# Performance work log

Measured on AMD Instinct MI355X. Metric: run time of the kernel, lower is better.

Reference implementation:

```python
import jax, jax.numpy as jnp
import numpy as np
import math

BS, C, H, W, D = 2, 64, 32, 16, 32
FLAT = H * W * D          # 16384 voxels
N = 2048                  # non-empty voxels per sample (fixed for jit)
K = 256                   # min(int(0.2 * N), max_k=256)
EPS = 1e-5


def _pe(c, length):
    # sinusoidal positional encoding, interleaved sin/cos as in the torch code
    pos = jnp.arange(length, dtype=jnp.float32)[:, None]
    div = jnp.exp(jnp.arange(0, c, 2, dtype=jnp.float32) * (-math.log(10000.0) / c))
    ang = pos * div[None, :]                     # [length, c//2]
    return jnp.stack([jnp.sin(ang), jnp.cos(ang)], axis=-1).reshape(length, c)


def _bn(z, g, b):
    # eval-mode BatchNorm1d with running_mean=0, running_var=1
    return z * (g / jnp.sqrt(1.0 + EPS)) + b


def setup_inputs() -> dict:
    key = jax.random.key(0)
    ks = jax.random.split(key, 8)
    rng = np.random.default_rng(0)
    mask_idx = np.stack([np.sort(rng.choice(FLAT, size=N, replace=False)) for _ in range(BS)])
    w = lambda k, s: jax.random.normal(k, s, jnp.float32) * 0.05
    return dict(
        input=jax.random.normal(ks[0], (BS, C, H, W, D), jnp.float32),
        mask_idx=jnp.asarray(mask_idx, jnp.int32),
        w_ne1=w(ks[1], (C, 32)), b_ne1=jnp.zeros(32), g_ne=jnp.ones(32), be_ne=jnp.zeros(32),
        w_ne2=w(ks[2], (32, 1)), b_ne2=jnp.zeros(1),
        w_p1=w(ks[3], (C, 32)), b_p1=jnp.zeros(32), g_p1=jnp.ones(32), be_p1=jnp.zeros(32),
        w_p2=w(ks[4], (32, 32)), b_p2=jnp.zeros(32), g_p2=jnp.ones(32), be_p2=jnp.zeros(32),
        w_p3=w(ks[5], (32, 1)), b_p3=jnp.zeros(1),
        w_r1=w(ks[6], (4 * C, 2 * C)), b_r1=jnp.zeros(2 * C),
        w_r2=w(ks[7], (2 * C, C)), b_r2=jnp.zeros(C),
    )


def reference(input, mask_idx, w_ne1, b_ne1, g_ne, be_ne, w_ne2, b_ne2,
              w_p1, b_p1, g_p1, be_p1, w_p2, b_p2, g_p2, be_p2, w_p3, b_p3,
              w_r1, b_r1, w_r2, b_r2):
    bs, c = input.shape[0], input.shape[1]
    pe = _pe(c, FLAT)
    x = input                         # agg (external Bottleneck3D stack) ~ identity
    x_flat = x.reshape(bs, c, FLAT)

    def per_sample(xf, idx, key):
        mpe = pe[idx]                                  # [N, c] masked positional enc
        xi = xf[:, idx].T + mpe                        # [N, c] masked gather
        h1 = jax.nn.relu(_bn(xi @ w_ne1 + b_ne1, g_ne, be_ne))
        prob = jax.nn.sigmoid((h1 @ w_ne2 + b_ne2)[:, 0])    # [N] non-empty prob
        # torch.multinomial(prob, K, replacement=True)
        topk = jax.random.categorical(key, jnp.log(prob), shape=(K,))
        tf = xi[topk]                                  # [K, c] sampled features
        ne_k = prob[topk]                              # [K]
        # xi_repeat + tiled masked_pe[topk]  ->  [N, K, c]
        xw = xi[:, None, :] + mpe[topk][None, :, :]
        hp = jax.nn.relu(_bn(xw @ w_p1 + b_p1, g_p1, be_p1))
        hp = jax.nn.relu(_bn(hp @ w_p2 + b_p2, g_p2, be_p2))
        P = jax.nn.sigmoid((hp @ w_p3 + b_p3)[..., 0])  # [N, K]
        Pi = P * ne_k[None, :]
        Pe_ = (1.0 - P) * ne_k[None, :]
        x_intra = (Pi @ tf) / jnp.sum(Pi, axis=1, keepdims=True)   # [N, c]
        x_inter = (Pe_ @ tf) / jnp.sum(Pe_, axis=1, keepdims=True)
        ctx = jnp.zeros((2 * c, FLAT), input.dtype)
        ctx = ctx.at[:c, idx].set(x_intra.T).at[c:, idx].set(x_inter.T)
        return ctx

    keys = jax.random.split(jax.random.key(42), bs)
    ctx = jax.vmap(per_sample)(x_flat, mask_idx, keys).reshape(bs, 2 * c, H, W, D)
    xcat = jnp.concatenate([input, ctx, x], axis=1)     # [bs, 4c, H, W, D]
    # resize: the two defined 1x1 Conv3d layers (Bottleneck3D blocks are external)
    y = jnp.einsum('bchwd,cf->bfhwd', xcat, w_r1) + b_r1[None, :, None, None, None]
    y = jnp.einsum('bchwd,cf->bfhwd', y, w_r2) + b_r2[None, :, None, None, None]
    return y
```

## Files before the change

### kernel.cpp

```cpp
#include <hip/hip_runtime.h>
#include <cstdint>
#include <cmath>

#define BS    2
#define CC    64
#define FLAT  16384
#define NN    2048
#define KK    256
#define EPSBN 1e-5f
#define TINYF 1.17549435e-38f
#define PE_SCALE -0.14391156831212787f
#define JAX_PARTITIONABLE 1

#define OFF_XI    0
#define OFF_XI1   (OFF_XI   + BS*NN*CC)
#define OFF_PROB  (OFF_XI1  + BS*NN*32)
#define OFF_LOGP  (OFF_PROB + BS*NN)
#define OFF_NEK   (OFF_LOGP + BS*NN)
#define OFF_TF    (OFF_NEK  + BS*KK)
#define OFF_M1    (OFF_TF   + BS*KK*CC)
#define OFF_DELTA (OFF_M1   + BS*KK*32)
#define OFF_WF    (OFF_DELTA+ BS*NN*CC)
#define OFF_BF    (OFF_WF   + 256*CC)
#define OFF_INV   (OFF_BF   + CC)

__device__ __forceinline__ uint32_t rotl32(uint32_t x, int r) {
  return (x << r) | (x >> (32 - r));
}
__device__ __forceinline__ void tf2x32(uint32_t k0, uint32_t k1,
                                       uint32_t& x0, uint32_t& x1) {
  uint32_t k2 = k0 ^ k1 ^ 0x1BD11BDAu;
  x0 += k0; x1 += k1;
#define TFR(r) { x0 += x1; x1 = rotl32(x1, r); x1 ^= x0; }
  TFR(13) TFR(15) TFR(26) TFR(6)  x0 += k1; x1 += k2 + 1u;
  TFR(17) TFR(29) TFR(16) TFR(24) x0 += k2; x1 += k0 + 2u;
  TFR(13) TFR(15) TFR(26) TFR(6)  x0 += k0; x1 += k1 + 3u;
  TFR(17) TFR(29) TFR(16) TFR(24) x0 += k1; x1 += k2 + 4u;
  TFR(13) TFR(15) TFR(26) TFR(6)  x0 += k2; x1 += k0 + 5u;
#undef TFR
}
__device__ __forceinline__ void jax_key(int b, uint32_t& k0, uint32_t& k1) {
#if JAX_PARTITIONABLE
  uint32_t x0 = 0u, x1 = (uint32_t)b;
  tf2x32(0u, 42u, x0, x1);
  k0 = x0; k1 = x1;
#else
  uint32_t a0 = 0u, a1 = 2u, c0 = 1u, c1 = 3u;
  tf2x32(0u, 42u, a0, a1);
  tf2x32(0u, 42u, c0, c1);
  if (b == 0) { k0 = a0; k1 = c0; } else { k0 = a1; k1 = c1; }
#endif
}
__device__ __forceinline__ uint32_t jax_bits(uint32_t k0, uint32_t k1, uint32_t i) {
#if JAX_PARTITIONABLE
  uint32_t x0 = 0u, x1 = i;
  tf2x32(k0, k1, x0, x1);
  return x0 ^ x1;
#else
  const uint32_t half = (uint32_t)(KK * NN) / 2u;
  uint32_t x0, x1;
  if (i < half) { x0 = i; x1 = i + half; tf2x32(k0, k1, x0, x1); return x0; }
  else          { x0 = i - half; x1 = i; tf2x32(k0, k1, x0, x1); return x1; }
#endif
}

__global__ void k0_fold(const float* __restrict__ w_r1, const float* __restrict__ b_r1,
                        const float* __restrict__ w_r2, const float* __restrict__ b_r2,
                        float* __restrict__ ws) {
  int c = blockIdx.x;
  int co = threadIdx.x;
  float acc = 0.f;
  for (int f = 0; f < 128; ++f)
    acc += w_r1[c * 128 + f] * w_r2[f * 64 + co];
  ws[OFF_WF + c * 64 + co] = acc;
  if (blockIdx.x == 0) {
    float bb = b_r2[co];
    for (int f = 0; f < 128; ++f) bb += b_r1[f] * w_r2[f * 64 + co];
    ws[OFF_BF + co] = bb;
  }
  int* inv = (int*)(ws + OFF_INV);
  int t = blockIdx.x * 64 + threadIdx.x;
  inv[t] = -1;
  inv[t + BS * FLAT / 2] = -1;
}

__global__ __launch_bounds__(256) void k1_xi(
    const float* __restrict__ input, const int* __restrict__ midx,
    const float* __restrict__ w_ne1, const float* __restrict__ b_ne1,
    const float* __restrict__ g_ne,  const float* __restrict__ be_ne,
    const float* __restrict__ w_ne2, const float* __restrict__ b_ne2,
    const float* __restrict__ w_p1,  const float* __restrict__ g_p1,
    float* __restrict__ ws) {
  int tid = threadIdx.x;
  int j = tid & 31, nl = tid >> 5;
  int bn = blockIdx.x * 8 + nl;
  int b = bn >> 11, n = bn & (NN - 1);
  int pos = midx[b * NN + n];
  __shared__ float xis[8][66];
  float d = expf((float)(2 * j) * PE_SCALE);
  float ang = (float)pos * d;
  float xs = sinf(ang) + input[((size_t)(b * CC + 2 * j)) * FLAT + pos];
  float xc = cosf(ang) + input[((size_t)(b * CC + 2 * j + 1)) * FLAT + pos];
  xis[nl][2 * j] = xs; xis[nl][2 * j + 1] = xc;
  float2 v2; v2.x = xs; v2.y = xc;
  ((float2*)(ws + OFF_XI + (size_t)(b * NN + n) * CC))[j] = v2;
  __syncthreads();
  float zne = b_ne1[j];
  float z1 = 0.f;
#pragma unroll
  for (int c2 = 0; c2 < CC; ++c2) {
    float xv = xis[nl][c2];
    zne += xv * w_ne1[c2 * 32 + j];
    z1  += xv * w_p1[c2 * 32 + j];
  }
  float ane = g_ne[j] / sqrtf(1.f + EPSBN);
  float h = fmaxf(0.f, zne * ane + be_ne[j]);
  float pp = h * w_ne2[j];
  for (int off = 16; off > 0; off >>= 1) pp += __shfl_down(pp, off, 32);
  if (j == 0) {
    float prob = 1.f / (1.f + expf(-(pp + b_ne2[0])));
    ws[OFF_PROB + b * NN + n] = prob;
    ws[OFF_LOGP + b * NN + n] = logf(prob);
    ((int*)(ws + OFF_INV))[b * FLAT + pos] = n;
  }
  float a1 = g_p1[j] / sqrtf(1.f + EPSBN);
  ws[OFF_XI1 + (size_t)(b * NN + n) * 32 + j] = z1 * a1;
}

__global__ __launch_bounds__(256) void k2_sample(
    const int* __restrict__ midx,
    const float* __restrict__ w_p1, const float* __restrict__ b_p1,
    const float* __restrict__ g_p1, const float* __restrict__ be_p1,
    float* __restrict__ ws) {
  int b = blockIdx.x >> 8, k = blockIdx.x & 255;
  int tid = threadIdx.x;
  uint32_t kb0, kb1;
  jax_key(b, kb0, kb1);
  const float* logp = ws + OFF_LOGP + b * NN;
  const float NEGINF = -__builtin_inff();
  float bv = NEGINF; int bn = NN;
#pragma unroll 1
  for (int r = 0; r < 8; ++r) {
    int n = r * 256 + tid;
    uint32_t bits = jax_bits(kb0, kb1, (uint32_t)(k * NN + n));
    float f = __uint_as_float(0x3f800000u | (bits >> 9)) - 1.0f;
    float u = fmaxf(TINYF, f + TINYF);
    float gmb = -logf(-logf(u));
    float v = logp[n] + gmb;
    if (v > bv || (v == bv && n < bn)) { bv = v; bn = n; }
  }
  __shared__ float sv[256];
  __shared__ int   sn[256];
  __shared__ float mpe[CC];
  sv[tid] = bv; sn[tid] = bn;
  __syncthreads();
  for (int s = 128; s > 0; s >>= 1) {
    if (tid < s) {
      float v2 = sv[tid + s]; int n2 = sn[tid + s];
      if (v2 > sv[tid] || (v2 == sv[tid] && n2 < sn[tid])) { sv[tid] = v2; sn[tid] = n2; }
    }
    __syncthreads();
  }
  int best = sn[0];
  if (tid == 0)
    ws[OFF_NEK + b * KK + k] = ws[OFF_PROB + b * NN + best];
  if (tid < CC) {
    int c = tid;
    ws[OFF_TF + (size_t)(b * KK + k) * CC + c] =
        ws[OFF_XI + (size_t)(b * NN + best) * CC + c];
    int pos = midx[b * NN + best];
    int jj = c >> 1;
    float ang = (float)pos * expf((float)(2 * jj) * PE_SCALE);
    mpe[c] = (c & 1) ? cosf(ang) : sinf(ang);
  }
  __syncthreads();
  if (tid < 32) {
    int jj = tid;
    float acc = b_p1[jj];
#pragma unroll
    for (int c = 0; c < CC; ++c) acc += mpe[c] * w_p1[c * 32 + jj];
    float a = g_p1[jj] / sqrtf(1.f + EPSBN);
    ws[OFF_M1 + (size_t)(b * KK + k) * 32 + jj] = acc * a + be_p1[jj];
  }
}

__global__ __launch_bounds__(256) void k3_pair(
    const float* __restrict__ w_p2, const float* __restrict__ b_p2,
    const float* __restrict__ g_p2, const float* __restrict__ be_p2,
    const float* __restrict__ w_p3, const float* __restrict__ b_p3,
    float* __restrict__ ws) {
  __shared__ __align__(16) float w2s[1024];
  __shared__ __align__(16) float m1t[32 * 264];
  __shared__ __align__(16) float PQT[8][256];
  __shared__ __align__(16) float xi1s[4][32];
  __shared__ __align__(16) float c2f[32];
  __shared__ __align__(16) float w3l[32];
  __shared__ __align__(16) float xIl[4 * 68], xEl[4 * 68];
  __shared__ float sI[4], sE[4];
  int tid = threadIdx.x;
  int b = blockIdx.x >> 9;
  int n0 = (blockIdx.x & 511) * 4;
  int kg = tid >> 3, qg = tid & 7;
  int k0 = kg * 8, q0 = qg * 4;
  {
    const float4* m4 = (const float4*)(ws + OFF_M1 + (size_t)(b * KK + tid) * 32);
#pragma unroll
    for (int q = 0; q < 8; ++q) {
      float4 v = m4[q];
      m1t[(q * 4 + 0) * 264 + tid] = v.x;
      m1t[(q * 4 + 1) * 264 + tid] = v.y;
      m1t[(q * 4 + 2) * 264 + tid] = v.z;
      m1t[(q * 4 + 3) * 264 + tid] = v.w;
    }
  }
  for (int e = tid; e < 1024; e += 256) {
    int jj = e & 31;
    w2s[e] = w_p2[e] * (g_p2[jj] / sqrtf(1.f + EPSBN));
  }
  if (tid < 32) {
    c2f[tid] = b_p2[tid] * (g_p2[tid] / sqrtf(1.f + EPSBN)) + be_p2[tid];
    w3l[tid] = w_p3[tid];
  }
  if (tid < 128) {
    int nn = tid >> 5, jx = tid & 31;
    xi1s[nn][jx] = ws[OFF_XI1 + (size_t)(b * NN + n0 + nn) * 32 + jx];
  }
  float nekv = ws[OFF_NEK + b * KK + tid];
  float b3 = b_p3[0];
  __syncthreads();
  const float4* w2s4 = (const float4*)w2s;
  const float4 cv = *(const float4*)&c2f[q0];
  const float4 w3v = *(const float4*)&w3l[q0];
#pragma unroll 1
  for (int nn = 0; nn < 4; ++nn) {
    float z[8][4];
#pragma unroll
    for (int i = 0; i < 8; ++i) {
      z[i][0] = cv.x; z[i][1] = cv.y; z[i][2] = cv.z; z[i][3] = cv.w;
    }
#pragma unroll 8
    for (int jj = 0; jj < 32; ++jj) {
      float xv = xi1s[nn][jj];
      float4 w = w2s4[jj * 8 + qg];
      const float4* mr = (const float4*)&m1t[jj * 264 + k0];
      float4 ma = mr[0], mb = mr[1];
      float h[8];
      h[0] = fmaxf(0.f, xv + ma.x); h[1] = fmaxf(0.f, xv + ma.y);
      h[2] = fmaxf(0.f, xv + ma.z); h[3] = fmaxf(0.f, xv + ma.w);
      h[4] = fmaxf(0.f, xv + mb.x); h[5] = fmaxf(0.f, xv + mb.y);
      h[6] = fmaxf(0.f, xv + mb.z); h[7] = fmaxf(0.f, xv + mb.w);
#pragma unroll
      for (int i = 0; i < 8; ++i) {
        z[i][0] += h[i] * w.x; z[i][1] += h[i] * w.y;
        z[i][2] += h[i] * w.z; z[i][3] += h[i] * w.w;
      }
    }
    float s[8];
#pragma unroll
    for (int i = 0; i < 8; ++i)
      s[i] = fmaxf(0.f, z[i][0]) * w3v.x + fmaxf(0.f, z[i][1]) * w3v.y
           + fmaxf(0.f, z[i][2]) * w3v.z + fmaxf(0.f, z[i][3]) * w3v.w;
#pragma unroll
    for (int i = 0; i < 8; ++i) {
      s[i] += __shfl_xor(s[i], 1, 64);
      s[i] += __shfl_xor(s[i], 2, 64);
      s[i] += __shfl_xor(s[i], 4, 64);
    }
    float sv = qg < 4 ? (qg < 2 ? (qg == 0 ? s[0] : s[1]) : (qg == 2 ? s[2] : s[3]))
                      : (qg < 6 ? (qg == 4 ? s[4] : s[5]) : (qg == 6 ? s[6] : s[7]));
    float P = 1.f / (1.f + expf(-(sv + b3)));
    PQT[nn * 2 + 0][tid] = P * nekv;
    PQT[nn * 2 + 1][tid] = (1.f - P) * nekv;
  }
  __syncthreads();
  if (tid < 128) {
    int nn = tid >> 5, jx = tid & 31;
    int pi = nn * 2;
    float s1 = 0.f, s2 = 0.f;
#pragma unroll
    for (int t = 0; t < 8; ++t) {
      s1 += PQT[pi][jx + 32 * t];
      s2 += PQT[pi + 1][jx + 32 * t];
    }
    for (int off = 16; off > 0; off >>= 1) {
      s1 += __shfl_down(s1, off, 32);
      s2 += __shfl_down(s2, off, 32);
    }
    if (jx == 0) { sI[nn] = s1; sE[nn] = s2; }
  }
  __syncthreads();
  {
    int c = tid & 63, n = tid >> 6;
    int pip = n * 2;
    const float4* PI4 = (const float4*)PQT[pip];
    const float4* PE4 = (const float4*)PQT[pip + 1];
    const float* tfg = ws + OFF_TF + (size_t)b * KK * CC + c;
    float aI = 0.f, aE = 0.f;
#pragma unroll 4
    for (int kq = 0; kq < 64; ++kq) {
      float4 piv = PI4[kq], pev = PE4[kq];
      float t0 = tfg[(4 * kq + 0) * 64];
      float t1 = tfg[(4 * kq + 1) * 64];
      float t2 = tfg[(4 * kq + 2) * 64];
      float t3 = tfg[(4 * kq + 3) * 64];
      aI += piv.x * t0 + piv.y * t1 + piv.z * t2 + piv.w * t3;
      aE += pev.x * t0 + pev.y * t1 + pev.z * t2 + pev.w * t3;
    }
    xIl[n * 68 + c] = aI / sI[n];
    xEl[n * 68 + c] = aE / sE[n];
  }
  __syncthreads();
  {
    int co = tid & 63, nn = tid >> 6;
    const float4* xI4 = (const float4*)&xIl[nn * 68];
    const float4* xE4 = (const float4*)&xEl[nn * 68];
    const float* wI = ws + OFF_WF + 64 * CC + co;
    const float* wE = ws + OFF_WF + 128 * CC + co;
    float dsum = 0.f;
#pragma unroll 4
    for (int cq = 0; cq < 16; ++cq) {
      float4 xi4 = xI4[cq], xe4 = xE4[cq];
      dsum += xi4.x * wI[(4 * cq + 0) * 64] + xi4.y * wI[(4 * cq + 1) * 64]
            + xi4.z * wI[(4 * cq + 2) * 64] + xi4.w * wI[(4 * cq + 3) * 64];
      dsum += xe4.x * wE[(4 * cq + 0) * 64] + xe4.y * wE[(4 * cq + 1) * 64]
            + xe4.z * wE[(4 * cq + 2) * 64] + xe4.w * wE[(4 * cq + 3) * 64];
    }
    ws[OFF_DELTA + (size_t)(b * NN + n0 + nn) * CC + co] = dsum;
  }
}

__global__ __launch_bounds__(256) void k4_out(
    const float* __restrict__ input, float* __restrict__ out,
    const float* __restrict__ ws) {
  __shared__ __align__(16) float wfa[64 * 64];
  __shared__ float bfl[64];
  int tid = threadIdx.x;
  const float* wf = ws + OFF_WF;
  for (int e = tid; e < 4096; e += 256) {
    int c = e >> 6, co = e & 63;
    wfa[e] = wf[c * 64 + co] + wf[(192 + c) * 64 + co];
  }
  if (tid < 64) bfl[tid] = ws[OFF_BF + tid];
  __syncthreads();
  int q = tid >> 6, lane = tid & 63;
  int pg = blockIdx.x * 64 + lane;
  int b = pg >> 14, pos = pg & (FLAT - 1);
  const int* inv = (const int*)(ws + OFF_INV);
  float acc[16];
#pragma unroll
  for (int u = 0; u < 16; ++u) acc[u] = bfl[q * 16 + u];
#pragma unroll 4
  for (int c = 0; c < 64; ++c) {
    float xv = input[((size_t)(b * CC + c)) * FLAT + pos];
    const float4* wr = (const float4*)&wfa[c * 64 + q * 16];
#pragma unroll
    for (int u4 = 0; u4 < 4; ++u4) {
      float4 w = wr[u4];
      acc[u4 * 4 + 0] += xv * w.x; acc[u4 * 4 + 1] += xv * w.y;
      acc[u4 * 4 + 2] += xv * w.z; acc[u4 * 4 + 3] += xv * w.w;
    }
  }
  int n = inv[pg];
  if (n >= 0) {
    const float4* dr = (const float4*)(ws + OFF_DELTA + (size_t)(b * NN + n) * CC + q * 16);
#pragma unroll
    for (int u4 = 0; u4 < 4; ++u4) {
      float4 dv = dr[u4];
      acc[u4 * 4 + 0] += dv.x; acc[u4 * 4 + 1] += dv.y;
      acc[u4 * 4 + 2] += dv.z; acc[u4 * 4 + 3] += dv.w;
    }
  }
#pragma unroll
  for (int u = 0; u < 16; ++u)
    out[((size_t)(b * CC + q * 16 + u)) * FLAT + pos] = acc[u];
}

extern "C" void kernel_launch(void* const* d_in, const int* in_sizes, int n_in,
                              void* d_out, int out_size, void* d_ws, size_t ws_size,
                              hipStream_t stream) {
  const float* input = (const float*)d_in[0];
  const int*   midx  = (const int*)  d_in[1];
  const float* w_ne1 = (const float*)d_in[2];
  const float* b_ne1 = (const float*)d_in[3];
  const float* g_ne  = (const float*)d_in[4];
  const float* be_ne = (const float*)d_in[5];
  const float* w_ne2 = (const float*)d_in[6];
  const float* b_ne2 = (const float*)d_in[7];
  const float* w_p1  = (const float*)d_in[8];
  const float* b_p1  = (const float*)d_in[9];
  const float* g_p1  = (const float*)d_in[10];
  const float* be_p1 = (const float*)d_in[11];
  const float* w_p2  = (const float*)d_in[12];
  const float* b_p2  = (const float*)d_in[13];
  const float* g_p2  = (const float*)d_in[14];
  const float* be_p2 = (const float*)d_in[15];
  const float* w_p3  = (const float*)d_in[16];
  const float* b_p3  = (const float*)d_in[17];
  const float* w_r1  = (const float*)d_in[18];
  const float* b_r1  = (const float*)d_in[19];
  const float* w_r2  = (const float*)d_in[20];
  const float* b_r2  = (const float*)d_in[21];
  float* out = (float*)d_out;
  float* ws  = (float*)d_ws;

  k0_fold<<<dim3(256), dim3(64), 0, stream>>>(w_r1, b_r1, w_r2, b_r2, ws);
  k1_xi<<<dim3(BS * NN / 8), dim3(256), 0, stream>>>(
      input, midx, w_ne1, b_ne1, g_ne, be_ne, w_ne2, b_ne2, w_p1, g_p1, ws);
  k2_sample<<<dim3(BS * KK), dim3(256), 0, stream>>>(
      midx, w_p1, b_p1, g_p1, be_p1, ws);
  k3_pair<<<dim3(BS * NN / 4), dim3(256), 0, stream>>>(
      w_p2, b_p2, g_p2, be_p2, w_p3, b_p3, ws);
  k4_out<<<dim3(BS * FLAT / 64), dim3(256), 0, stream>>>(input, out, ws);
}
```

Measured before the change: 192.1 us.

## Split pair kernel into probability and context kernels, precompute ReLU hidden in LDS

The fused pair kernel is split in two. The first kernel computes P*ne_k per (n,k) and writes it to a new global workspace buffer, storing each thread's m1 row in registers and building the ReLU'd layer-1 activations in LDS per point. This removes the repeated add+max per FMA group in the inner loop. The second kernel reads P back, derives the inter weights as ne_k - Pi instead of keeping a second array, and does the weighted tf reductions. This adds a global round trip of BS*NN*KK floats, one extra launch and extra barriers per point, and the workspace must be large enough for the new OFF_PP region.

```diff
diff --git a/kernel.cpp b/kernel.cpp
--- a/kernel.cpp
+++ b/kernel.cpp
@@ -23,6 +23,7 @@
 #define OFF_WF    (OFF_DELTA+ BS*NN*CC)
 #define OFF_BF    (OFF_WF   + 256*CC)
 #define OFF_INV   (OFF_BF   + CC)
+#define OFF_PP    (OFF_INV  + BS*FLAT)
 
 __device__ __forceinline__ uint32_t rotl32(uint32_t x, int r) {
   return (x << r) | (x >> (32 - r));
@@ -184,103 +185,115 @@
   }
 }
 
-__global__ __launch_bounds__(256) void k3_pair(
+__global__ __launch_bounds__(256) void k3a_pairP(
     const float* __restrict__ w_p2, const float* __restrict__ b_p2,
     const float* __restrict__ g_p2, const float* __restrict__ be_p2,
     const float* __restrict__ w_p3, const float* __restrict__ b_p3,
     float* __restrict__ ws) {
   __shared__ __align__(16) float w2s[1024];
-  __shared__ __align__(16) float m1t[32 * 264];
-  __shared__ __align__(16) float PQT[8][256];
+  __shared__ __align__(16) float hbuf[32 * 264];
   __shared__ __align__(16) float xi1s[4][32];
   __shared__ __align__(16) float c2f[32];
   __shared__ __align__(16) float w3l[32];
+  int tid = threadIdx.x;
+  int b = blockIdx.x >> 9;
+  int n0 = (blockIdx.x & 511) * 4;
+  int kg = tid >> 3, qg = tid & 7;
+  int k0 = kg * 8, q0 = qg * 4;
+  float m1r[32];
+  {
+    const float4* m4 = (const float4*)(ws + OFF_M1 + (size_t)(b * KK + tid) * 32);
+#pragma unroll
+    for (int q = 0; q < 8; ++q) {
+      float4 v = m4[q];
+      m1r[q * 4 + 0] = v.x; m1r[q * 4 + 1] = v.y;
+      m1r[q * 4 + 2] = v.z; m1r[q * 4 + 3] = v.w;
+    }
+  }
+  for (int e = tid; e < 1024; e += 256) {
+    int jj = e & 31;
+    w2s[e] = w_p2[e] * (g_p2[jj] / sqrtf(1.f + EPSBN));
+  }
+  if (tid < 32) {
+    c2f[tid] = b_p2[tid] * (g_p2[tid] / sqrtf(1.f + EPSBN)) + be_p2[tid];
+    w3l[tid] = w_p3[tid];
+  }
+  if (tid < 128) {
+    int nn = tid >> 5, jx = tid & 31;
+    xi1s[nn][jx] = ws[OFF_XI1 + (size_t)(b * NN + n0 + nn) * 32 + jx];
+  }
+  float nekv = ws[OFF_NEK + b * KK + tid];
+  float b3 = b_p3[0];
+  __syncthreads();
+  const float4* w2s4 = (const float4*)w2s;
+  const float4 cv = *(const float4*)&c2f[q0];
+  const float4 w3v = *(const float4*)&w3l[q0];
+#pragma unroll 1
+  for (int nn = 0; nn < 4; ++nn) {
+#pragma unroll
+    for (int j = 0; j < 32; ++j)
+      hbuf[j * 264 + tid] = fmaxf(0.f, xi1s[nn][j] + m1r[j]);
+    __syncthreads();
+    float z[8][4];
+#pragma unroll
+    for (int i = 0; i < 8; ++i) {
+      z[i][0] = cv.x; z[i][1] = cv.y; z[i][2] = cv.z; z[i][3] = cv.w;
+    }
+#pragma unroll 8
+    for (int jj = 0; jj < 32; ++jj) {
+      float4 w = w2s4[jj * 8 + qg];
+      const float4* mr = (const float4*)&hbuf[jj * 264 + k0];
+      float4 ha = mr[0], hb = mr[1];
+      z[0][0] += ha.x * w.x; z[0][1] += ha.x * w.y; z[0][2] += ha.x * w.z; z[0][3] += ha.x * w.w;
+      z[1][0] += ha.y * w.x; z[1][1] += ha.y * w.y; z[1][2] += ha.y * w.z; z[1][3] += ha.y * w.w;
+      z[2][0] += ha.z * w.x; z[2][1] += ha.z * w.y; z[2][2] += ha.z * w.z; z[2][3] += ha.z * w.w;
+      z[3][0] += ha.w * w.x; z[3][1] += ha.w * w.y; z[3][2] += ha.w * w.z; z[3][3] += ha.w * w.w;
+      z[4][0] += hb.x * w.x; z[4][1] += hb.x * w.y; z[4][2] += hb.x * w.z; z[4][3] += hb.x * w.w;
+      z[5][0] += hb.y * w.x; z[5][1] += hb.y * w.y; z[5][2] += hb.y * w.z; z[5][3] += hb.y * w.w;
+      z[6][0] += hb.z * w.x; z[6][1] += hb.z * w.y; z[6][2] += hb.z * w.z; z[6][3] += hb.z * w.w;
+      z[7][0] += hb.w * w.x; z[7][1] += hb.w * w.y; z[7][2] += hb.w * w.z; z[7][3] += hb.w * w.w;
+    }
+    float s[8];
+#pragma unroll
+    for (int i = 0; i < 8; ++i)
+      s[i] = fmaxf(0.f, z[i][0]) * w3v.x + fmaxf(0.f, z[i][1]) * w3v.y
+           + fmaxf(0.f, z[i][2]) * w3v.z + fmaxf(0.f, z[i][3]) * w3v.w;
+#pragma unroll
+    for (int i = 0; i < 8; ++i) {
+      s[i] += __shfl_xor(s[i], 1, 64);
+      s[i] += __shfl_xor(s[i], 2, 64);
+      s[i] += __shfl_xor(s[i], 4, 64);
+    }
+    float sv = qg < 4 ? (qg < 2 ? (qg == 0 ? s[0] : s[1]) : (qg == 2 ? s[2] : s[3]))
+                      : (qg < 6 ? (qg == 4 ? s[4] : s[5]) : (qg == 6 ? s[6] : s[7]));
+    float P = 1.f / (1.f + expf(-(sv + b3)));
+    ws[OFF_PP + (size_t)(b * NN + n0 + nn) * KK + tid] = P * nekv;
+    __syncthreads();
+  }
+}
+
+__global__ __launch_bounds__(256) void k3b_ctx(
+    float* __restrict__ ws) {
+  __shared__ __align__(16) float Pis[4][256];
+  __shared__ __align__(16) float nekl[256];
   __shared__ __align__(16) float xIl[4 * 68], xEl[4 * 68];
   __shared__ float sI[4], sE[4];
   int tid = threadIdx.x;
   int b = blockIdx.x >> 9;
   int n0 = (blockIdx.x & 511) * 4;
-  int kg = tid >> 3, qg = tid & 7;
-  int k0 = kg * 8, q0 = qg * 4;
-  {
-    const float4* m4 = (const float4*)(ws + OFF_M1 + (size_t)(b * KK + tid) * 32);
-#pragma unroll
-    for (int q = 0; q < 8; ++q) {
-      float4 v = m4[q];
-      m1t[(q * 4 + 0) * 264 + tid] = v.x;
-      m1t[(q * 4 + 1) * 264 + tid] = v.y;
-      m1t[(q * 4 + 2) * 264 + tid] = v.z;
-      m1t[(q * 4 + 3) * 264 + tid] = v.w;
-    }
-  }
-  for (int e = tid; e < 1024; e += 256) {
-    int jj = e & 31;
-    w2s[e] = w_p2[e] * (g_p2[jj] / sqrtf(1.f + EPSBN));
-  }
-  if (tid < 32) {
-    c2f[tid] = b_p2[tid] * (g_p2[tid] / sqrtf(1.f + EPSBN)) + be_p2[tid];
-    w3l[tid] = w_p3[tid];
-  }
+#pragma unroll
+  for (int e = 0; e < 4; ++e)
+    Pis[e][tid] = ws[OFF_PP + (size_t)(b * NN + n0 + e) * KK + tid];
+  nekl[tid] = ws[OFF_NEK + b * KK + tid];
+  __syncthreads();
   if (tid < 128) {
     int nn = tid >> 5, jx = tid & 31;
-    xi1s[nn][jx] = ws[OFF_XI1 + (size_t)(b * NN + n0 + nn) * 32 + jx];
-  }
-  float nekv = ws[OFF_NEK + b * KK + tid];
-  float b3 = b_p3[0];
-  __syncthreads();
-  const float4* w2s4 = (const float4*)w2s;
-  const float4 cv = *(const float4*)&c2f[q0];
-  const float4 w3v = *(const float4*)&w3l[q0];
-#pragma unroll 1
-  for (int nn = 0; nn < 4; ++nn) {
-    float z[8][4];
-#pragma unroll
-    for (int i = 0; i < 8; ++i) {
-      z[i][0] = cv.x; z[i][1] = cv.y; z[i][2] = cv.z; z[i][3] = cv.w;
-    }
-#pragma unroll 8
-    for (int jj = 0; jj < 32; ++jj) {
-      float xv = xi1s[nn][jj];
-      float4 w = w2s4[jj * 8 + qg];
-      const float4* mr = (const float4*)&m1t[jj * 264 + k0];
-      float4 ma = mr[0], mb = mr[1];
-      float h[8];
-      h[0] = fmaxf(0.f, xv + ma.x); h[1] = fmaxf(0.f, xv + ma.y);
-      h[2] = fmaxf(0.f, xv + ma.z); h[3] = fmaxf(0.f, xv + ma.w);
-      h[4] = fmaxf(0.f, xv + mb.x); h[5] = fmaxf(0.f, xv + mb.y);
-      h[6] = fmaxf(0.f, xv + mb.z); h[7] = fmaxf(0.f, xv + mb.w);
-#pragma unroll
-      for (int i = 0; i < 8; ++i) {
-        z[i][0] += h[i] * w.x; z[i][1] += h[i] * w.y;
-        z[i][2] += h[i] * w.z; z[i][3] += h[i] * w.w;
-      }
-    }
-    float s[8];
-#pragma unroll
-    for (int i = 0; i < 8; ++i)
-      s[i] = fmaxf(0.f, z[i][0]) * w3v.x + fmaxf(0.f, z[i][1]) * w3v.y
-           + fmaxf(0.f, z[i][2]) * w3v.z + fmaxf(0.f, z[i][3]) * w3v.w;
-#pragma unroll
-    for (int i = 0; i < 8; ++i) {
-      s[i] += __shfl_xor(s[i], 1, 64);
-      s[i] += __shfl_xor(s[i], 2, 64);
-      s[i] += __shfl_xor(s[i], 4, 64);
-    }
-    float sv = qg < 4 ? (qg < 2 ? (qg == 0 ? s[0] : s[1]) : (qg == 2 ? s[2] : s[3]))
-                      : (qg < 6 ? (qg == 4 ? s[4] : s[5]) : (qg == 6 ? s[6] : s[7]));
-    float P = 1.f / (1.f + expf(-(sv + b3)));
-    PQT[nn * 2 + 0][tid] = P * nekv;
-    PQT[nn * 2 + 1][tid] = (1.f - P) * nekv;
-  }
-  __syncthreads();
-  if (tid < 128) {
-    int nn = tid >> 5, jx = tid & 31;
-    int pi = nn * 2;
     float s1 = 0.f, s2 = 0.f;
 #pragma unroll
     for (int t = 0; t < 8; ++t) {
-      s1 += PQT[pi][jx + 32 * t];
-      s2 += PQT[pi + 1][jx + 32 * t];
+      float pi = Pis[nn][jx + 32 * t];
+      s1 += pi;
+      s2 += nekl[jx + 32 * t] - pi;
     }
     for (int off = 16; off > 0; off >>= 1) {
       s1 += __shfl_down(s1, off, 32);
@@ -291,20 +304,20 @@
   __syncthreads();
   {
     int c = tid & 63, n = tid >> 6;
-    int pip = n * 2;
-    const float4* PI4 = (const float4*)PQT[pip];
-    const float4* PE4 = (const float4*)PQT[pip + 1];
+    const float4* PI4 = (const float4*)Pis[n];
+    const float4* NE4 = (const float4*)nekl;
     const float* tfg = ws + OFF_TF + (size_t)b * KK * CC + c;
     float aI = 0.f, aE = 0.f;
 #pragma unroll 4
     for (int kq = 0; kq < 64; ++kq) {
-      float4 piv = PI4[kq], pev = PE4[kq];
+      float4 piv = PI4[kq], nev = NE4[kq];
       float t0 = tfg[(4 * kq + 0) * 64];
       float t1 = tfg[(4 * kq + 1) * 64];
       float t2 = tfg[(4 * kq + 2) * 64];
       float t3 = tfg[(4 * kq + 3) * 64];
       aI += piv.x * t0 + piv.y * t1 + piv.z * t2 + piv.w * t3;
-      aE += pev.x * t0 + pev.y * t1 + pev.z * t2 + pev.w * t3;
+      aE += (nev.x - piv.x) * t0 + (nev.y - piv.y) * t1
+          + (nev.z - piv.z) * t2 + (nev.w - piv.w) * t3;
     }
     xIl[n * 68 + c] = aI / sI[n];
     xEl[n * 68 + c] = aE / sE[n];
@@ -408,7 +421,8 @@
       input, midx, w_ne1, b_ne1, g_ne, be_ne, w_ne2, b_ne2, w_p1, g_p1, ws);
   k2_sample<<<dim3(BS * KK), dim3(256), 0, stream>>>(
       midx, w_p1, b_p1, g_p1, be_p1, ws);
-  k3_pair<<<dim3(BS * NN / 4), dim3(256), 0, stream>>>(
+  k3a_pairP<<<dim3(BS * NN / 4), dim3(256), 0, stream>>>(
       w_p2, b_p2, g_p2, be_p2, w_p3, b_p3, ws);
+  k3b_ctx<<<dim3(BS * NN / 4), dim3(256), 0, stream>>>(ws);
   k4_out<<<dim3(BS * FLAT / 64), dim3(256), 0, stream>>>(input, out, ws);
 }
```

Measured after the change: 190.9 us. Within noise of the previous version (-0.6%).
